# Performance work log

Hardware: AMD Instinct MI355X
Metric: run time of the kernel (lower is better)

The kernel has to match this reference:

```python
import jax, jax.numpy as jnp
import numpy as np

LMAX, MMAX = 6, 2
C, COUT = 64, 64
E = 50000


def _perms():
    # l-primary coefficient order: for l in 0..lmax, m in -min(l,mmax)..min(l,mmax)
    lp = [(l, m) for l in range(LMAX + 1) for m in range(-min(l, MMAX), min(l, MMAX) + 1)]
    # m-primary order: m=0 block, then for each m>0: real (+m) block then imag (-m) block
    mp = [(l, 0) for l in range(LMAX + 1)]
    for m in range(1, MMAX + 1):
        mp += [(l, m) for l in range(m, LMAX + 1)]
        mp += [(l, -m) for l in range(m, LMAX + 1)]
    to_m = np.array([lp.index(p) for p in mp])   # gather: l-primary -> m-primary
    from_m = np.argsort(to_m)                    # inverse gather: m-primary -> l-primary
    return to_m, from_m

TO_M, FROM_M = _perms()


def setup_inputs() -> dict:
    key = jax.random.key(0)
    ks = jax.random.split(key, 6)
    sz0 = LMAX + 1                      # m_size[0] = 7
    in0 = sz0 * C                       # fc_m0 in_features = 448
    out0 = COUT * sz0                   # fc_m0 out_features = 448
    sz1, sz2 = LMAX, LMAX - 1           # m_size[1]=6, m_size[2]=5
    inp = {
        "x_embedding": jax.random.normal(ks[0], (E, len(TO_M), C), dtype=jnp.float32),
        "x_edge": jax.random.normal(ks[1], (E, 1), dtype=jnp.float32),
        "W0": jax.random.normal(ks[2], (out0, in0), dtype=jnp.float32) / np.sqrt(in0),
        "b0": jnp.zeros((out0,), dtype=jnp.float32),
        "W1": jax.random.normal(ks[3], (2 * COUT * sz1, sz1 * C), dtype=jnp.float32) / np.sqrt(2 * sz1 * C),
        "W2": jax.random.normal(ks[4], (2 * COUT * sz2, sz2 * C), dtype=jnp.float32) / np.sqrt(2 * sz2 * C),
    }
    return inp


def reference(x_embedding, x_edge, W0, b0, W1, W2):
    num_edges = x_embedding.shape[0]
    # _m_primary: permute coefficients to m-primary layout
    x = x_embedding[:, TO_M, :]                         # [E, 29, C]
    out = []
    # m = 0 path (fc_m0 with bias)
    sz0 = LMAX + 1
    x0 = x[:, :sz0, :].reshape(num_edges, sz0 * C)
    x0 = x0 @ W0.T + b0                                 # [E, sz0*COUT]
    out.append(x0.reshape(num_edges, sz0, COUT))
    # m = 1..mmax: SO2_m_Convolution (complex multiply structure)
    offset = sz0
    for m, Wm in zip(range(1, MMAX + 1), (W1, W2)):
        sz = LMAX - m + 1
        xm = x[:, offset:offset + 2 * sz, :].reshape(num_edges, 2, sz * C)
        y = jnp.einsum('enk,ok->eno', xm, Wm)           # [E, 2, 2*sz*COUT]
        half = sz * COUT
        x_r, x_i = y[..., :half], y[..., half:]
        x_m_r = x_r[:, 0:1] - x_i[:, 1:2]
        x_m_i = x_r[:, 1:2] + x_i[:, 0:1]
        xm_out = jnp.concatenate((x_m_r, x_m_i), axis=1)  # [E, 2, sz*COUT]
        out.append(xm_out.reshape(num_edges, 2 * sz, COUT))
        offset += 2 * sz
    out = jnp.concatenate(out, axis=1)                  # [E, 29, COUT] m-primary
    # _l_primary: back to l-primary layout
    return out[:, FROM_M, :]
```

## Files before the change

kernel.cpp:

```cpp
#include <hip/hip_runtime.h>
#include <hip/hip_bf16.h>

typedef __attribute__((ext_vector_type(8))) short short8;
typedef __attribute__((ext_vector_type(4))) float f32x4;
typedef __attribute__((ext_vector_type(4))) unsigned int uint4v;

#define NROW 29
#define CCH 64
#define XSTRIDE 1856
#define N0SQ (448*448)
#define N1SQ (768*768)
#define N2SQ (640*640)

__constant__ int d_TO_M[29] = {0,2,6,11,16,21,26, 3,7,12,17,22,27, 1,5,10,15,20,25,
                               8,13,18,23,28, 4,9,14,19,24};

__device__ __forceinline__ short f2bf(float f) {
    __hip_bfloat16 h = __float2bfloat16(f);
    return __builtin_bit_cast(short, h);
}

__device__ __forceinline__ void wg_barrier() {
    asm volatile("s_waitcnt lgkmcnt(0)" ::: "memory");
    __builtin_amdgcn_s_barrier();
    __builtin_amdgcn_sched_barrier(0);
}

__global__ __launch_bounds__(256) void prep_weights(const float* __restrict__ W0,
                                                    const float* __restrict__ W1,
                                                    const float* __restrict__ W2,
                                                    short* __restrict__ ws) {
    int idx = blockIdx.x * 256 + threadIdx.x;
    if (idx < N0SQ) {
        ws[idx] = f2bf(W0[idx]);
        return;
    }
    idx -= N0SQ;
    if (idx < N1SQ) {
        int n = idx / 768, k = idx % 768;
        int no = n / 384, ni = n % 384;
        int ko = k / 384, ki = k % 384;
        float v;
        if (no == ko)      v =  W1[ni * 384 + ki];
        else if (no == 0)  v = -W1[(384 + ni) * 384 + ki];
        else               v =  W1[(384 + ni) * 384 + ki];
        ws[N0SQ + idx] = f2bf(v);
        return;
    }
    idx -= N1SQ;
    if (idx < N2SQ) {
        int n = idx / 640, k = idx % 640;
        int no = n / 320, ni = n % 320;
        int ko = k / 320, ki = k % 320;
        float v;
        if (no == ko)      v =  W2[ni * 320 + ki];
        else if (no == 0)  v = -W2[(320 + ni) * 320 + ki];
        else               v =  W2[(320 + ni) * 320 + ki];
        ws[N0SQ + N1SQ + idx] = f2bf(v);
    }
}

__global__ __launch_bounds__(256) void so2_gemm(const float* __restrict__ x,
                                                const float* __restrict__ b0,
                                                const short* __restrict__ wsW,
                                                float* __restrict__ out,
                                                int E, int nwg) {
    int orig = blockIdx.x;
    int q8 = nwg >> 3, r8 = nwg & 7;
    int xcd = orig & 7, pos = orig >> 3;
    int wgid = (xcd < r8 ? xcd * (q8 + 1) : r8 * (q8 + 1) + (xcd - r8) * q8) + pos;

    int etile = wgid / 15;
    int ncol  = wgid % 15;
    int blk, ntl;
    if (ncol < 4)       { blk = 0; ntl = ncol; }
    else if (ncol < 10) { blk = 1; ntl = ncol - 4; }
    else                { blk = 2; ntl = ncol - 10; }
    const int Kb     = (blk == 0) ? 448 : (blk == 1) ? 768 : 640;
    const int ksteps = Kb >> 5;
    const int kbase  = (blk == 0) ? 0 : (blk == 1) ? 7 : 19;
    const int nrows  = (blk == 0) ? 7 : (blk == 1) ? 12 : 10;
    const long woff  = (blk == 0) ? 0 : (blk == 1) ? (long)N0SQ : (long)(N0SQ + N1SQ);
    const short* Wb  = wsW + woff;

    __shared__ short Alds[2][128 * 32];
    __shared__ short Blds[2][128 * 32];

    const int tid  = threadIdx.x;
    const int w    = tid >> 6, lane = tid & 63;
    const int wr   = w >> 1,   wc   = w & 1;
    const int lrow = lane & 15, lk  = lane >> 4;
    const int ebase = etile * 128;

    const int qr = tid >> 2;
    const int rq = tid & 3;

    const int e1 = ebase + qr,      e2 = ebase + 64 + qr;
    const bool eok1 = e1 < E,       eok2 = e2 < E;
    const int n1 = ntl * 128 + qr,  n2 = n1 + 64;
    const bool nok1 = n1 < Kb,      nok2 = n2 < Kb;

    const float* xb1 = x + (size_t)e1 * XSTRIDE + rq * 8;
    const float* xb2 = x + (size_t)e2 * XSTRIDE + rq * 8;
    const short* wb1 = Wb + (size_t)n1 * Kb + rq * 8;
    const short* wb2 = Wb + (size_t)n2 * Kb + rq * 8;

    f32x4 acc[4][4] = {};

    f32x4 sA0[4], sA1[4];
    uint4v sB[2];

    auto issueA = [&](int kt, f32x4* ar) {
        int g = d_TO_M[kbase + (kt >> 1)];
        size_t off = (size_t)g * CCH + (size_t)((kt & 1) * 32);
        if (eok1) { ar[0] = *(const f32x4*)(xb1 + off); ar[1] = *(const f32x4*)(xb1 + off + 4); }
        else      { ar[0] = f32x4{0,0,0,0};             ar[1] = f32x4{0,0,0,0}; }
        if (eok2) { ar[2] = *(const f32x4*)(xb2 + off); ar[3] = *(const f32x4*)(xb2 + off + 4); }
        else      { ar[2] = f32x4{0,0,0,0};             ar[3] = f32x4{0,0,0,0}; }
    };
    auto issueB = [&](int kt) {
        int off = kt * 32;
        sB[0] = nok1 ? *(const uint4v*)(wb1 + off) : uint4v{0,0,0,0};
        sB[1] = nok2 ? *(const uint4v*)(wb2 + off) : uint4v{0,0,0,0};
    };
    auto writeL = [&](int pb, const f32x4* ar) {
        short8 h0, h1;
#pragma unroll
        for (int j = 0; j < 4; ++j) {
            h0[j]     = f2bf(ar[0][j]);  h0[4 + j] = f2bf(ar[1][j]);
            h1[j]     = f2bf(ar[2][j]);  h1[4 + j] = f2bf(ar[3][j]);
        }
        *(short8*)&Alds[pb][qr * 32 + rq * 8]        = h0;
        *(short8*)&Alds[pb][(64 + qr) * 32 + rq * 8] = h1;
        *(uint4v*)&Blds[pb][qr * 32 + rq * 8]        = sB[0];
        *(uint4v*)&Blds[pb][(64 + qr) * 32 + rq * 8] = sB[1];
    };
    auto compute = [&](int pb) {
        short8 af[4], bf[4];
#pragma unroll
        for (int mf = 0; mf < 4; ++mf)
            af[mf] = *(short8*)&Alds[pb][(wr * 64 + mf * 16 + lrow) * 32 + lk * 8];
#pragma unroll
        for (int nf = 0; nf < 4; ++nf)
            bf[nf] = *(short8*)&Blds[pb][(wc * 64 + nf * 16 + lrow) * 32 + lk * 8];
#pragma unroll
        for (int mf = 0; mf < 4; ++mf)
#pragma unroll
            for (int nf = 0; nf < 4; ++nf)
                acc[mf][nf] = __builtin_amdgcn_mfma_f32_16x16x32_bf16(af[mf], bf[nf], acc[mf][nf], 0, 0, 0);
    };

    issueA(0, sA0); issueB(0);
    issueA(1, sA1);
    writeL(0, sA0);
    issueB(1);
    issueA(2, sA0);
    wg_barrier();

    for (int kt = 0; kt < ksteps; kt += 2) {
        compute(0);
        writeL(1, sA1);
        if (kt + 2 < ksteps) {
            issueB(kt + 2);
            issueA(kt + 3, sA1);
        }
        wg_barrier();
        compute(1);
        if (kt + 2 < ksteps) {
            writeL(0, sA0);
            issueB(kt + 3);
            if (kt + 4 < ksteps) issueA(kt + 4, sA0);
        }
        wg_barrier();
    }

    int mrow_l = ntl * 2 + wc;
    if (mrow_l < nrows) {
        int lp = d_TO_M[kbase + mrow_l];
        float* op = out + (size_t)lp * CCH;
#pragma unroll
        for (int nf = 0; nf < 4; ++nf) {
            int c = nf * 16 + lrow;
            float bias = 0.f;
            if (blk == 0) bias = b0[mrow_l * 64 + c];
#pragma unroll
            for (int mf = 0; mf < 4; ++mf) {
                int e0 = ebase + wr * 64 + mf * 16 + lk * 4;
#pragma unroll
                for (int j = 0; j < 4; ++j) {
                    int e = e0 + j;
                    if (e < E) op[(size_t)e * XSTRIDE + c] = acc[mf][nf][j] + bias;
                }
            }
        }
    }
}

extern "C" void kernel_launch(void* const* d_in, const int* in_sizes, int n_in,
                              void* d_out, int out_size, void* d_ws, size_t ws_size,
                              hipStream_t stream) {
    const float* x_emb = (const float*)d_in[0];
    const float* W0 = (const float*)d_in[2];
    const float* b0 = (const float*)d_in[3];
    const float* W1 = (const float*)d_in[4];
    const float* W2 = (const float*)d_in[5];
    float* out = (float*)d_out;
    short* ws  = (short*)d_ws;

    const int E = in_sizes[0] / (NROW * CCH);

    const int prep_total = N0SQ + N1SQ + N2SQ;
    prep_weights<<<(prep_total + 255) / 256, 256, 0, stream>>>(W0, W1, W2, ws);

    const int etiles = (E + 127) / 128;
    const int nwg = etiles * 15;
    so2_gemm<<<nwg, 256, 0, stream>>>(x_emb, b0, (const short*)ws, out, E, nwg);
}
```

Baseline: 419.1 us.

## Stage GEMM tiles via direct global-to-LDS loads with swizzled triple-buffered A

Replaces register-staged global loads and LDS writes with global_load_lds direct copies into XOR-swizzled shared memory. A is kept in fp32 in a three-stage LDS ring and converted to bf16 at fragment-read time. B is double-buffered, and the loop advances one k-step per iteration with a single vmcnt-gated barrier. W0 is padded to 512 rows so B loads need no bounds checks, and launch bounds request 2 waves per SIMD. This frees registers and overlaps loads with MFMA. The cost is more LDS use, since fp32 A doubles its footprint, and conversion work moves into the compute loop.

```diff
diff --git a/kernel.cpp b/kernel.cpp
--- a/kernel.cpp
+++ b/kernel.cpp
@@ -3,14 +3,12 @@
 
 typedef __attribute__((ext_vector_type(8))) short short8;
 typedef __attribute__((ext_vector_type(4))) float f32x4;
-typedef __attribute__((ext_vector_type(4))) unsigned int uint4v;
-
-#define NROW 29
+
+#define XSTRIDE 1856
 #define CCH 64
-#define XSTRIDE 1856
-#define N0SQ (448*448)
-#define N1SQ (768*768)
-#define N2SQ (640*640)
+#define OFF1 229376
+#define OFF2 819200
+#define WTOT 1228800
 
 __constant__ int d_TO_M[29] = {0,2,6,11,16,21,26, 3,7,12,17,22,27, 1,5,10,15,20,25,
                                8,13,18,23,28, 4,9,14,19,24};
@@ -20,10 +18,9 @@
     return __builtin_bit_cast(short, h);
 }
 
-__device__ __forceinline__ void wg_barrier() {
-    asm volatile("s_waitcnt lgkmcnt(0)" ::: "memory");
-    __builtin_amdgcn_s_barrier();
-    __builtin_amdgcn_sched_barrier(0);
+__device__ __forceinline__ void load16_lds(const void* g, void* l) {
+    __builtin_amdgcn_global_load_lds((const __attribute__((address_space(1))) unsigned int*)g,
+                                     (__attribute__((address_space(3))) unsigned int*)l, 16, 0, 0);
 }
 
 __global__ __launch_bounds__(256) void prep_weights(const float* __restrict__ W0,
@@ -31,40 +28,40 @@
                                                     const float* __restrict__ W2,
                                                     short* __restrict__ ws) {
     int idx = blockIdx.x * 256 + threadIdx.x;
-    if (idx < N0SQ) {
-        ws[idx] = f2bf(W0[idx]);
+    if (idx < OFF1) {
+        ws[idx] = (idx < 448 * 448) ? f2bf(W0[idx]) : (short)0;
         return;
     }
-    idx -= N0SQ;
-    if (idx < N1SQ) {
-        int n = idx / 768, k = idx % 768;
+    if (idx < OFF2) {
+        int i = idx - OFF1;
+        int n = i / 768, k = i % 768;
         int no = n / 384, ni = n % 384;
-        int ko = k / 384, ki = k % 384;
+        int ki = k % 384;
         float v;
-        if (no == ko)      v =  W1[ni * 384 + ki];
-        else if (no == 0)  v = -W1[(384 + ni) * 384 + ki];
-        else               v =  W1[(384 + ni) * 384 + ki];
-        ws[N0SQ + idx] = f2bf(v);
+        if (no == (k / 384)) v =  W1[ni * 384 + ki];
+        else if (no == 0)    v = -W1[(384 + ni) * 384 + ki];
+        else                 v =  W1[(384 + ni) * 384 + ki];
+        ws[idx] = f2bf(v);
         return;
     }
-    idx -= N1SQ;
-    if (idx < N2SQ) {
-        int n = idx / 640, k = idx % 640;
+    if (idx < WTOT) {
+        int i = idx - OFF2;
+        int n = i / 640, k = i % 640;
         int no = n / 320, ni = n % 320;
-        int ko = k / 320, ki = k % 320;
+        int ki = k % 320;
         float v;
-        if (no == ko)      v =  W2[ni * 320 + ki];
-        else if (no == 0)  v = -W2[(320 + ni) * 320 + ki];
-        else               v =  W2[(320 + ni) * 320 + ki];
-        ws[N0SQ + N1SQ + idx] = f2bf(v);
-    }
-}
-
-__global__ __launch_bounds__(256) void so2_gemm(const float* __restrict__ x,
-                                                const float* __restrict__ b0,
-                                                const short* __restrict__ wsW,
-                                                float* __restrict__ out,
-                                                int E, int nwg) {
+        if (no == (k / 320)) v =  W2[ni * 320 + ki];
+        else if (no == 0)    v = -W2[(320 + ni) * 320 + ki];
+        else                 v =  W2[(320 + ni) * 320 + ki];
+        ws[idx] = f2bf(v);
+    }
+}
+
+__global__ __launch_bounds__(256, 2) void so2_gemm_f(const float* __restrict__ x,
+                                                     const float* __restrict__ b0,
+                                                     const short* __restrict__ wsW,
+                                                     float* __restrict__ out,
+                                                     int E, int nwg) {
     int orig = blockIdx.x;
     int q8 = nwg >> 3, r8 = nwg & 7;
     int xcd = orig & 7, pos = orig >> 3;
@@ -80,11 +77,12 @@
     const int ksteps = Kb >> 5;
     const int kbase  = (blk == 0) ? 0 : (blk == 1) ? 7 : 19;
     const int nrows  = (blk == 0) ? 7 : (blk == 1) ? 12 : 10;
-    const long woff  = (blk == 0) ? 0 : (blk == 1) ? (long)N0SQ : (long)(N0SQ + N1SQ);
+    const long woff  = (blk == 0) ? 0 : (blk == 1) ? (long)OFF1 : (long)OFF2;
     const short* Wb  = wsW + woff;
-
-    __shared__ short Alds[2][128 * 32];
-    __shared__ short Blds[2][128 * 32];
+    const int n0 = ntl * 128;
+
+    __shared__ float Af[3][128 * 32];
+    __shared__ short Bf[2][128 * 32];
 
     const int tid  = threadIdx.x;
     const int w    = tid >> 6, lane = tid & 63;
@@ -92,57 +90,55 @@
     const int lrow = lane & 15, lk  = lane >> 4;
     const int ebase = etile * 128;
 
-    const int qr = tid >> 2;
-    const int rq = tid & 3;
-
-    const int e1 = ebase + qr,      e2 = ebase + 64 + qr;
-    const bool eok1 = e1 < E,       eok2 = e2 < E;
-    const int n1 = ntl * 128 + qr,  n2 = n1 + 64;
-    const bool nok1 = n1 < Kb,      nok2 = n2 < Kb;
-
-    const float* xb1 = x + (size_t)e1 * XSTRIDE + rq * 8;
-    const float* xb2 = x + (size_t)e2 * XSTRIDE + rq * 8;
-    const short* wb1 = Wb + (size_t)n1 * Kb + rq * 8;
-    const short* wb2 = Wb + (size_t)n2 * Kb + rq * 8;
+    const int lr = lane >> 3;
+    const int ca = (lane & 7) ^ lr;
+    const int rbq = lane >> 2;
+    const int cb = (lane & 3) ^ ((lane >> 3) & 3);
 
     f32x4 acc[4][4] = {};
 
-    f32x4 sA0[4], sA1[4];
-    uint4v sB[2];
-
-    auto issueA = [&](int kt, f32x4* ar) {
+    auto stageA = [&](int kt, int pb) {
         int g = d_TO_M[kbase + (kt >> 1)];
-        size_t off = (size_t)g * CCH + (size_t)((kt & 1) * 32);
-        if (eok1) { ar[0] = *(const f32x4*)(xb1 + off); ar[1] = *(const f32x4*)(xb1 + off + 4); }
-        else      { ar[0] = f32x4{0,0,0,0};             ar[1] = f32x4{0,0,0,0}; }
-        if (eok2) { ar[2] = *(const f32x4*)(xb2 + off); ar[3] = *(const f32x4*)(xb2 + off + 4); }
-        else      { ar[2] = f32x4{0,0,0,0};             ar[3] = f32x4{0,0,0,0}; }
+        const float* src = x + (size_t)g * CCH + (kt & 1) * 32 + ca * 4;
+#pragma unroll
+        for (int j = 0; j < 4; ++j) {
+            int rb = w * 32 + j * 8;
+            int e = ebase + rb + lr;
+            if (e >= E) e = E - 1;
+            load16_lds(src + (size_t)e * XSTRIDE,
+                       (char*)&Af[pb][rb * 32] + lane * 16);
+        }
     };
-    auto issueB = [&](int kt) {
-        int off = kt * 32;
-        sB[0] = nok1 ? *(const uint4v*)(wb1 + off) : uint4v{0,0,0,0};
-        sB[1] = nok2 ? *(const uint4v*)(wb2 + off) : uint4v{0,0,0,0};
+    auto stageB = [&](int kt, int pb) {
+        const short* src = Wb + (size_t)kt * 32 + cb * 8;
+#pragma unroll
+        for (int j = 0; j < 2; ++j) {
+            int rb = w * 32 + j * 16;
+            int n = n0 + rb + rbq;
+            load16_lds(src + (size_t)n * Kb,
+                       (char*)&Bf[pb][rb * 32] + lane * 16);
+        }
     };
-    auto writeL = [&](int pb, const f32x4* ar) {
-        short8 h0, h1;
-#pragma unroll
-        for (int j = 0; j < 4; ++j) {
-            h0[j]     = f2bf(ar[0][j]);  h0[4 + j] = f2bf(ar[1][j]);
-            h1[j]     = f2bf(ar[2][j]);  h1[4 + j] = f2bf(ar[3][j]);
-        }
-        *(short8*)&Alds[pb][qr * 32 + rq * 8]        = h0;
-        *(short8*)&Alds[pb][(64 + qr) * 32 + rq * 8] = h1;
-        *(uint4v*)&Blds[pb][qr * 32 + rq * 8]        = sB[0];
-        *(uint4v*)&Blds[pb][(64 + qr) * 32 + rq * 8] = sB[1];
-    };
-    auto compute = [&](int pb) {
+    auto compute = [&](int pa, int pbb) {
         short8 af[4], bf[4];
 #pragma unroll
-        for (int mf = 0; mf < 4; ++mf)
-            af[mf] = *(short8*)&Alds[pb][(wr * 64 + mf * 16 + lrow) * 32 + lk * 8];
-#pragma unroll
-        for (int nf = 0; nf < 4; ++nf)
-            bf[nf] = *(short8*)&Blds[pb][(wc * 64 + nf * 16 + lrow) * 32 + lk * 8];
+        for (int mf = 0; mf < 4; ++mf) {
+            int r = wr * 64 + mf * 16 + lrow;
+            int s0 = (2 * lk) ^ (lrow & 7);
+            int s1 = (2 * lk + 1) ^ (lrow & 7);
+            f32x4 lo = *(const f32x4*)&Af[pa][r * 32 + s0 * 4];
+            f32x4 hi = *(const f32x4*)&Af[pa][r * 32 + s1 * 4];
+            short8 v;
+#pragma unroll
+            for (int j = 0; j < 4; ++j) { v[j] = f2bf(lo[j]); v[4 + j] = f2bf(hi[j]); }
+            af[mf] = v;
+        }
+#pragma unroll
+        for (int nf = 0; nf < 4; ++nf) {
+            int r = wc * 64 + nf * 16 + lrow;
+            int s = lk ^ ((lrow >> 1) & 3);
+            bf[nf] = *(const short8*)&Bf[pbb][r * 32 + s * 8];
+        }
 #pragma unroll
         for (int mf = 0; mf < 4; ++mf)
 #pragma unroll
@@ -150,28 +146,29 @@
                 acc[mf][nf] = __builtin_amdgcn_mfma_f32_16x16x32_bf16(af[mf], bf[nf], acc[mf][nf], 0, 0, 0);
     };
 
-    issueA(0, sA0); issueB(0);
-    issueA(1, sA1);
-    writeL(0, sA0);
-    issueB(1);
-    issueA(2, sA0);
-    wg_barrier();
-
-    for (int kt = 0; kt < ksteps; kt += 2) {
-        compute(0);
-        writeL(1, sA1);
+    stageA(0, 0);
+    stageB(0, 0);
+    stageA(1, 1);
+    asm volatile("s_waitcnt vmcnt(4)" ::: "memory");
+    __builtin_amdgcn_s_barrier();
+    __builtin_amdgcn_sched_barrier(0);
+
+    int pa = 0;
+    for (int kt = 0; kt < ksteps; ++kt) {
+        int pa1 = pa + 1; if (pa1 == 3) pa1 = 0;
+        int pa2 = pa1 + 1; if (pa2 == 3) pa2 = 0;
+        if (kt + 1 < ksteps) stageB(kt + 1, (kt + 1) & 1);
+        __builtin_amdgcn_sched_barrier(0);
+        if (kt + 2 < ksteps) stageA(kt + 2, pa2);
+        compute(pa, kt & 1);
         if (kt + 2 < ksteps) {
-            issueB(kt + 2);
-            issueA(kt + 3, sA1);
-        }
-        wg_barrier();
-        compute(1);
-        if (kt + 2 < ksteps) {
-            writeL(0, sA0);
-            issueB(kt + 3);
-            if (kt + 4 < ksteps) issueA(kt + 4, sA0);
-        }
-        wg_barrier();
+            asm volatile("s_waitcnt vmcnt(4)" ::: "memory");
+        } else if (kt + 1 < ksteps) {
+            asm volatile("s_waitcnt vmcnt(0)" ::: "memory");
+        }
+        __builtin_amdgcn_s_barrier();
+        __builtin_amdgcn_sched_barrier(0);
+        pa = pa1;
     }
 
     int mrow_l = ntl * 2 + wc;
@@ -207,12 +204,10 @@
     float* out = (float*)d_out;
     short* ws  = (short*)d_ws;
 
-    const int E = in_sizes[0] / (NROW * CCH);
-
-    const int prep_total = N0SQ + N1SQ + N2SQ;
-    prep_weights<<<(prep_total + 255) / 256, 256, 0, stream>>>(W0, W1, W2, ws);
-
+    const int E = in_sizes[0] / (29 * CCH);
     const int etiles = (E + 127) / 128;
     const int nwg = etiles * 15;
-    so2_gemm<<<nwg, 256, 0, stream>>>(x_emb, b0, (const short*)ws, out, E, nwg);
-}
+
+    prep_weights<<<(WTOT + 255) / 256, 256, 0, stream>>>(W0, W1, W2, ws);
+    so2_gemm_f<<<nwg, 256, 0, stream>>>(x_emb, b0, (const short*)ws, out, E, nwg);
+}
```

After: 452.7 us. 1.08x slower.
